# Kernel optimization log

Measured on AMD Instinct MI355X. Metric: run time of the kernel, lower is better.

Reference implementation:

```python
import jax, jax.numpy as jnp
import numpy as np

MAX_GRAD = 200.0
N_BLOCKS = 8

@jax.custom_jvp
def sqrt_bound(x):
    return jnp.sqrt(x)

@sqrt_bound.defjvp
def _sqrt_bound_jvp(primals, tangents):
    (x,), (xd,) = primals, tangents
    clipped = jnp.maximum(x, 1.0 / (4.0 * MAX_GRAD * MAX_GRAD))
    return jnp.sqrt(x), xd / (2.0 * jnp.sqrt(clipped))

def block_diag_linear(x, W, b):
    # x: [B,S,Din], W: [n_blocks, Din/n, Dout/n], b: [Dout]
    B, S, Din = x.shape
    n, blk_in, blk_out = W.shape
    xb = x.reshape(B, S, n, blk_in)
    y = jnp.einsum('bsnh,nhd->bsnd', xb, W).reshape(B, S, n * blk_out)
    return y + b

def _scan_combine(c1, c2):
    a1r, a1i, x1r, x1i = c1
    a2r, a2i, x2r, x2i = c2
    ar = a2r * a1r - a2i * a1i
    ai = a2r * a1i + a2i * a1r
    xr = a2r * x1r - a2i * x1i + x2r
    xi = a2r * x1i + a2i * x1r + x2i
    return (ar, ai, xr, xi)

def rglru_forward(x, a_real_param, a_imag_param, W_in, b_in, Wg_x, bg_x, Wg_a, bg_a, W_out, b_out):
    # x: [B, S, d_in]
    x_h = jnp.einsum('bsd,dh->bsh', x, W_in) + b_in          # [B,S,d_hidden]
    gate_x = jax.nn.sigmoid(block_diag_linear(x_h, Wg_x, bg_x))  # [B,S,Dh]
    gate_a = jax.nn.sigmoid(block_diag_linear(x_h, Wg_a, bg_a))  # [B,S,Dh]
    log_a = -8.0 * gate_a * jax.nn.softplus(a_real_param)        # Re(log a)
    log_a_imag = a_imag_param * gate_a                           # Im(log a)
    mag = jnp.exp(log_a)
    a_re = mag * jnp.cos(log_a_imag)
    a_im = mag * jnp.sin(log_a_imag)
    a_sq = jnp.exp(2.0 * log_a)                                  # |a|^2
    Dh = log_a.shape[-1]
    # merged_to_complex: first half -> real part, second half -> imag part
    xr = x_h[..., :Dh]
    xi = x_h[..., Dh:]
    xr = gate_x * xr
    xi = gate_x * xi
    norm = sqrt_bound(1.0 - a_sq)                                # input normalization
    xr = norm * xr
    xi = norm * xi
    # linear recurrence h_t = a_t * h_{t-1} + x_t  (h0 = 0), parallel scan over seq axis
    _, _, hr, hi = jax.lax.associative_scan(_scan_combine, (a_re, a_im, xr, xi), axis=1)
    h = jnp.concatenate([hr, hi], axis=-1)                       # complex_to_merged
    h_last = jnp.concatenate([hr[:, -1], hi[:, -1]], axis=-1)    # [B, d_hidden]
    y = jnp.einsum('bsh,hd->bsd', h, W_out) + b_out              # Dense(d_in)
    return y, h_last

def setup_inputs() -> dict:
    key = jax.random.key(0)
    ks = jax.random.split(key, 10)
    B, S, d_in, d_hidden = 4, 4096, 2048, 2048
    Dh = d_hidden // 2
    blk_in, blk_out = d_hidden // N_BLOCKS, Dh // N_BLOCKS
    r_min, r_max, max_imag, eps = 0.9, 0.999, 0.1, 1e-8
    u1 = jax.random.uniform(ks[0], (Dh,))
    a_real = 0.5 * jnp.log(u1 * (r_max**2 - r_min**2) + r_min**2 + eps)
    a_real_param = jnp.log(jnp.exp(-a_real) - 1.0)
    a_imag_param = jnp.pi * max_imag * jax.random.uniform(ks[1], (Dh,))
    x = jax.random.normal(ks[2], (B, S, d_in), dtype=jnp.float32)
    W_in = jax.random.normal(ks[3], (d_in, d_hidden)) / np.sqrt(d_in)
    Wg_x = jax.random.normal(ks[4], (N_BLOCKS, blk_in, blk_out)) / np.sqrt(blk_in)
    Wg_a = jax.random.normal(ks[5], (N_BLOCKS, blk_in, blk_out)) / np.sqrt(blk_in)
    W_out = jax.random.normal(ks[6], (d_hidden, d_in)) / np.sqrt(d_hidden)
    return {
        'x': x,
        'a_real_param': a_real_param.astype(jnp.float32),
        'a_imag_param': a_imag_param.astype(jnp.float32),
        'W_in': W_in.astype(jnp.float32), 'b_in': jnp.zeros((d_hidden,), jnp.float32),
        'Wg_x': Wg_x.astype(jnp.float32), 'bg_x': jnp.zeros((Dh,), jnp.float32),
        'Wg_a': Wg_a.astype(jnp.float32), 'bg_a': jnp.zeros((Dh,), jnp.float32),
        'W_out': W_out.astype(jnp.float32), 'b_out': jnp.zeros((d_in,), jnp.float32),
    }

def reference(x, a_real_param, a_imag_param, W_in, b_in, Wg_x, bg_x, Wg_a, bg_a, W_out, b_out):
    return rglru_forward(x, a_real_param, a_imag_param, W_in, b_in, Wg_x, bg_x, Wg_a, bg_a, W_out, b_out)
```

## Files before the change

kernel.cpp:

```cpp
#include <hip/hip_runtime.h>
#include <hip/hip_bf16.h>


typedef unsigned short u16;
typedef unsigned int u32;
typedef unsigned long long u64;
typedef __attribute__((ext_vector_type(8))) short short8;
typedef __attribute__((ext_vector_type(4))) float floatx4;

#define DEV __device__ __forceinline__

DEV float bf2f(u16 u) { union { u32 i; float f; } v; v.i = ((u32)u) << 16; return v.f; }
DEV u16 f2bf(float f) {
  union { float f; u32 i; } v; v.f = f;
  u32 r = v.i + 0x7fffu + ((v.i >> 16) & 1u);
  return (u16)(r >> 16);
}
DEV float sigmoidf_(float x) { return 1.f / (1.f + __expf(-x)); }

#if __has_builtin(__builtin_amdgcn_global_load_lds)
#define USE_ASYNC_LDS 1
#endif

DEV void cp16(const void* g, void* l) {
#if defined(USE_ASYNC_LDS) && defined(__HIP_DEVICE_COMPILE__)
  __builtin_amdgcn_global_load_lds((const __attribute__((address_space(1))) u32*)g,
                                   (__attribute__((address_space(3))) u32*)l, 16, 0, 0);
#else
  *(short8*)l = *(const short8*)g;
#endif
}
#define WAIT_VM() asm volatile("s_waitcnt vmcnt(0)" ::: "memory")
#define LGKM0()  do { asm volatile("s_waitcnt lgkmcnt(0)" ::: "memory"); __builtin_amdgcn_sched_barrier(0); } while (0)
#define BAR()    __builtin_amdgcn_s_barrier()
#define VMC4()   asm volatile("s_waitcnt vmcnt(4)" ::: "memory")
#define SETP(p)  __builtin_amdgcn_s_setprio(p)

__global__ __launch_bounds__(256) void convert_f32_bf16(
    const float* __restrict__ src, u16* __restrict__ dst, long n) {
  long i = ((long)blockIdx.x * 256 + threadIdx.x) * 8;
  if (i >= n) return;
  float4 a = *(const float4*)(src + i);
  float4 b = *(const float4*)(src + i + 4);
  union { u16 u[8]; short8 v; } o;
  o.u[0] = f2bf(a.x); o.u[1] = f2bf(a.y); o.u[2] = f2bf(a.z); o.u[3] = f2bf(a.w);
  o.u[4] = f2bf(b.x); o.u[5] = f2bf(b.y); o.u[6] = f2bf(b.z); o.u[7] = f2bf(b.w);
  *(short8*)(dst + i) = o.v;
}

__global__ __launch_bounds__(256) void transpose_f32_bf16(
    const float* __restrict__ src, u16* __restrict__ dst, int R, int C,
    long sBatch, long dBatch) {
  __shared__ u16 tile[32][33];
  const int n = blockIdx.z;
  src += (long)n * sBatch;
  dst += (long)n * dBatch;
  const int c0 = blockIdx.x * 32, r0 = blockIdx.y * 32;
  const int tx = threadIdx.x, ty = threadIdx.y;
#pragma unroll
  for (int i = 0; i < 32; i += 8)
    tile[ty + i][tx] = f2bf(src[(long)(r0 + ty + i) * C + c0 + tx]);
  __syncthreads();
#pragma unroll
  for (int i = 0; i < 32; i += 8) dst[(long)(c0 + ty + i) * R + r0 + tx] = tile[tx][ty + i];
}

#define MQK(MH, NH)                                                                  \
  {                                                                                  \
    _Pragma("unroll") for (int mi = 0; mi < 4; ++mi)                                 \
        _Pragma("unroll") for (int nj = 0; nj < 2; ++nj)                             \
      acc[(MH)*4 + mi][(NH)*2 + nj] = __builtin_amdgcn_mfma_f32_16x16x32_bf16(       \
          af[(MH)*4 + mi][0], bf[(NH)*2 + nj][0], acc[(MH)*4 + mi][(NH)*2 + nj],     \
          0, 0, 0);                                                                  \
    _Pragma("unroll") for (int mi = 0; mi < 4; ++mi)                                 \
        _Pragma("unroll") for (int nj = 0; nj < 2; ++nj)                             \
      acc[(MH)*4 + mi][(NH)*2 + nj] = __builtin_amdgcn_mfma_f32_16x16x32_bf16(       \
          af[(MH)*4 + mi][1], bf[(NH)*2 + nj][1], acc[(MH)*4 + mi][(NH)*2 + nj],     \
          0, 0, 0);                                                                  \
  }

#define RDA(m0_, BO)                                                                 \
  {                                                                                  \
    _Pragma("unroll") for (int mi = (m0_); mi < (m0_) + 4; ++mi) {                   \
      af[mi][0] = *(const short8*)((const char*)SM + ((aRd0 ^ (BO)) + mi * 2048));   \
      af[mi][1] = *(const short8*)((const char*)SM + ((aRd1 ^ (BO)) + mi * 2048));   \
    }                                                                                \
  }
#define RDB(n0_, BO)                                                                 \
  {                                                                                  \
    _Pragma("unroll") for (int nj = (n0_); nj < (n0_) + 2; ++nj) {                   \
      bf[nj][0] = *(const short8*)((const char*)SM + ((bRd0 ^ (BO)) + nj * 2048));   \
      bf[nj][1] = *(const short8*)((const char*)SM + ((bRd1 ^ (BO)) + nj * 2048));   \
    }                                                                                \
  }

template <typename OutT, int KK>
__global__ __launch_bounds__(512, 2) void gemm256_bt_bias(
    const u16* __restrict__ A, const u16* __restrict__ BT,
    const float* __restrict__ bias, OutT* __restrict__ C, int M, int N) {
  constexpr int NT = KK >> 6;
  __shared__ __align__(16) u16 SM[65536];
  const int mt = M >> 8;
  const int cpx = gridDim.x >> 3;
  const int bid = blockIdx.x;
  const int wg = (bid & 7) * cpx + (bid >> 3);
  const int bm = wg % mt, bn = wg / mt;
  const int m0 = bm << 8, n0 = bn << 8;
  const int tid = threadIdx.x;
  const int lane = tid & 63, wid = tid >> 6;
  const int wr = wid >> 2, wc = wid & 3;
  const int lq = lane >> 4, lm = lane & 15;
  const int sz = lm & 7;

  u32 goffA0, goffA1, goffB0, goffB1;
  u32 lofA0, lofA1, lofB0, lofB1;
  {
    const int rowl = tid >> 3, gch = (tid & 7) ^ (rowl & 7);
    goffA0 = (u32)(((size_t)(m0 + rowl) * KK + (gch << 3)) * 2);
    goffA1 = (u32)(((size_t)(m0 + 128 + rowl) * KK + (gch << 3)) * 2);
    goffB0 = (u32)(((size_t)(n0 + rowl) * KK + (gch << 3)) * 2);
    goffB1 = (u32)(((size_t)(n0 + 128 + rowl) * KK + (gch << 3)) * 2);
    const u32 sl = (u32)tid * 16;
    lofA0 = sl; lofA1 = sl + 16384; lofB0 = sl + 65536; lofB1 = sl + 81920;
  }
  const u32 aRd0 = (u32)((((wr << 7) + lm) << 7) + ((lq ^ sz) << 4));
  const u32 aRd1 = aRd0 ^ 64u;
  const u32 bRd0 = (u32)(65536 + (((wc << 6) + lm) << 7) + ((lq ^ sz) << 4));
  const u32 bRd1 = bRd0 ^ 64u;

  auto stage2 = [&](u32 go, const char* base, u32 lo, u32 bo) {
    cp16(base + go, (char*)SM + (lo ^ bo));
    cp16(base + go + 64 * KK * 2, (char*)SM + ((lo ^ bo) + 8192));
  };
#define SBA(t) ((const char*)A + ((size_t)(t) << 7))
#define SBB(t) ((const char*)BT + ((size_t)(t) << 7))

  floatx4 acc[8][4];
#pragma unroll
  for (int i = 0; i < 8; ++i)
#pragma unroll
    for (int j = 0; j < 4; ++j) { acc[i][j].x = 0.f; acc[i][j].y = 0.f; acc[i][j].z = 0.f; acc[i][j].w = 0.f; }
  short8 af[8][2], bf[4][2];

  stage2(goffA0, SBA(0), lofA0, 0);
  stage2(goffB0, SBB(0), lofB0, 0);
  stage2(goffA1, SBA(0), lofA1, 0);
  stage2(goffB1, SBB(0), lofB1, 0);
  stage2(goffA0, SBA(1), lofA0, 0x8000u);
  stage2(goffB0, SBB(1), lofB0, 0x8000u);
  stage2(goffA1, SBA(1), lofA1, 0x8000u);
  asm volatile("s_waitcnt vmcnt(6)" ::: "memory");
  BAR();
  RDA(0, 0u);
  RDB(0, 0u);

  for (int T = 0; T < NT - 2; ++T) {
    const u32 bo = (u32)((T & 1) << 15), bq = bo ^ 0x8000u;
    stage2(goffB1, SBB(T + 1), lofB1, bq);
    BAR(); LGKM0();
    RDB(2, bo);
    SETP(1); MQK(0, 0); SETP(0);
    BAR();
    stage2(goffA0, SBA(T + 2), lofA0, bo);
    BAR(); LGKM0();
    RDA(4, bo);
    SETP(1); MQK(0, 1); SETP(0);
    VMC4();
    BAR();
    stage2(goffB0, SBB(T + 2), lofB0, bo);
    BAR(); LGKM0();
    RDA(0, bq);
    SETP(1); MQK(1, 0); SETP(0);
    VMC4();
    BAR();
    stage2(goffA1, SBA(T + 2), lofA1, bo);
    BAR(); LGKM0();
    RDB(0, bq);
    SETP(1); MQK(1, 1); SETP(0);
    BAR();
  }
  {
    const int T = NT - 2;
    const u32 bo = (u32)((T & 1) << 15), bq = bo ^ 0x8000u;
    stage2(goffB1, SBB(T + 1), lofB1, bq);
    BAR(); LGKM0(); RDB(2, bo); SETP(1); MQK(0, 0); SETP(0); BAR();
    BAR(); LGKM0(); RDA(4, bo); SETP(1); MQK(0, 1); SETP(0); WAIT_VM(); BAR();
    BAR(); LGKM0(); RDA(0, bq); SETP(1); MQK(1, 0); SETP(0); BAR();
    BAR(); LGKM0(); RDB(0, bq); SETP(1); MQK(1, 1); SETP(0); BAR();
  }
  {
    const u32 bo = (u32)(((NT - 1) & 1) << 15);
    BAR(); LGKM0(); RDB(2, bo); SETP(1); MQK(0, 0); SETP(0); BAR();
    BAR(); LGKM0(); RDA(4, bo); SETP(1); MQK(0, 1); SETP(0); BAR();
    BAR(); LGKM0(); SETP(1); MQK(1, 0); SETP(0); BAR();
    BAR(); LGKM0(); SETP(1); MQK(1, 1); SETP(0); BAR();
  }
#undef SBA
#undef SBB

  float bv[4];
#pragma unroll
  for (int nj = 0; nj < 4; ++nj) bv[nj] = bias[n0 + (wc << 6) + nj * 16 + lm];
  float* Cs = (float*)SM;
#pragma unroll
  for (int s = 0; s < 4; ++s) {
    __syncthreads();
    if (wr == (s >> 1)) {
#pragma unroll
      for (int mi2 = 0; mi2 < 4; ++mi2) {
        const int mi = ((s & 1) << 2) + mi2;
#pragma unroll
        for (int nj = 0; nj < 4; ++nj)
#pragma unroll
          for (int rr = 0; rr < 4; ++rr)
            Cs[(mi2 * 16 + lq * 4 + rr) * 260 + (wc << 6) + nj * 16 + lm] =
                acc[mi][nj][rr] + bv[nj];
      }
    }
    __syncthreads();
#pragma unroll
    for (int w = 0; w < 8; ++w) {
      int fi = (w << 9) + tid;
      int rl = fi >> 6, cc = fi & 63;
      float4 v = *(const float4*)&Cs[rl * 260 + (cc << 2)];
      size_t grow = (size_t)(m0 + (s << 6) + rl) * N + n0 + (cc << 2);
      if constexpr (sizeof(OutT) == 2) {
        union { u16 u[4]; u64 q; } o;
        o.u[0] = f2bf(v.x); o.u[1] = f2bf(v.y); o.u[2] = f2bf(v.z); o.u[3] = f2bf(v.w);
        *(u64*)((u16*)C + grow) = o.q;
      } else {
        *(float4*)((float*)C + grow) = v;
      }
    }
  }
}

__global__ __launch_bounds__(256, 2) void gate_elem_kernel(
    const u16* __restrict__ xh, const u16* __restrict__ wgt,
    const float* __restrict__ bgx, const float* __restrict__ bga,
    const float* __restrict__ arp,
    float* __restrict__ ga_out, u16* __restrict__ xr_out, u16* __restrict__ xi_out) {
  __shared__ __align__(16) u16 As[128 * 64];
  __shared__ __align__(16) u16 Bs[256 * 64];

  const int m0 = blockIdx.x << 7;
  const int blk = blockIdx.y;
  const int tid = threadIdx.x;
  const int lane = tid & 63, wid = tid >> 6;
  const int wm = (wid & 1) << 6, wn = (wid >> 1) << 6;
  const int lq = lane >> 4, lm = lane & 15;

  floatx4 acc[4][8];
#pragma unroll
  for (int i = 0; i < 4; ++i)
#pragma unroll
    for (int j = 0; j < 8; ++j) { acc[i][j].x = 0.f; acc[i][j].y = 0.f; acc[i][j].z = 0.f; acc[i][j].w = 0.f; }

  const u16* Ag = xh + (size_t)m0 * 2048 + blk * 256;
  const u16* Bg = wgt + (size_t)blk * 65536;

  for (int kt = 0; kt < 256; kt += 64) {
#pragma unroll
    for (int j = 0; j < 4; ++j) {
      int slot = (j << 8) + tid;
      int row = slot >> 3, ch = slot & 7;
      int gch = ch ^ (row & 7);
      cp16(Ag + (size_t)row * 2048 + kt + (gch << 3), (char*)As + slot * 16);
    }
#pragma unroll
    for (int j = 0; j < 8; ++j) {
      int slot = (j << 8) + tid;
      int row = slot >> 3, ch = slot & 7;
      int gch = ch ^ (row & 7);
      cp16(Bg + (size_t)row * 256 + kt + (gch << 3), (char*)Bs + slot * 16);
    }
    WAIT_VM();
    __syncthreads();
#pragma unroll
    for (int kk = 0; kk < 64; kk += 32) {
      const int lc = (kk >> 3) + lq;
      short8 af[4], bfr[8];
#pragma unroll
      for (int mi = 0; mi < 4; ++mi) {
        int r = wm + mi * 16 + lm;
        af[mi] = *(const short8*)&As[r * 64 + ((lc ^ (r & 7)) << 3)];
      }
#pragma unroll
      for (int ni = 0; ni < 8; ++ni) {
        int r = (ni < 4) ? (wn + ni * 16 + lm) : (128 + wn + (ni - 4) * 16 + lm);
        bfr[ni] = *(const short8*)&Bs[r * 64 + ((lc ^ (r & 7)) << 3)];
      }
#pragma unroll
      for (int mi = 0; mi < 4; ++mi)
#pragma unroll
        for (int ni = 0; ni < 8; ++ni)
          acc[mi][ni] = __builtin_amdgcn_mfma_f32_16x16x32_bf16(af[mi], bfr[ni], acc[mi][ni], 0, 0, 0);
    }
    __syncthreads();
  }

#pragma unroll
  for (int ni = 0; ni < 4; ++ni) {
    const int c = (blk << 7) + wn + ni * 16 + lm;
    const float bxv = bgx[c], bav = bga[c];
    const float sp = log1pf(__expf(arp[c]));
#pragma unroll
    for (int mi = 0; mi < 4; ++mi) {
      const size_t rowg0 = (size_t)m0 + wm + mi * 16 + lq * 4;
#pragma unroll
      for (int r = 0; r < 4; ++r) {
        const size_t rowg = rowg0 + r;
        float gxv = sigmoidf_(acc[mi][ni][r] + bxv);
        float gav = sigmoidf_(acc[mi][ni + 4][r] + bav);
        float mag = __expf(-8.f * gav * sp);
        float norm = sqrtf(fmaxf(1.f - mag * mag, 0.f));
        float f = norm * gxv;
        ga_out[rowg * 1024 + c] = gav;
        xr_out[rowg * 1024 + c] = f2bf(f * bf2f(xh[rowg * 2048 + c]));
        xi_out[rowg * 1024 + c] = f2bf(f * bf2f(xh[rowg * 2048 + 1024 + c]));
      }
    }
  }
}

__global__ __launch_bounds__(256) void scan_pass1(
    const float* __restrict__ ga, const u16* __restrict__ xr, const u16* __restrict__ xi,
    const float* __restrict__ arp, const float* __restrict__ aip,
    float* __restrict__ Ar, float* __restrict__ Ai,
    float* __restrict__ Xr, float* __restrict__ Xi) {
  int tid = blockIdx.x * 256 + threadIdx.x;
  int c = tid & 1023;
  int chunk = (tid >> 10) & 63;
  int b = tid >> 16;
  float sp = log1pf(__expf(arp[c]));
  float aim = aip[c];
  size_t base = ((size_t)b * 4096 + chunk * 64) * 1024 + c;
  float Arr = 1.f, Aii = 0.f, Xrr = 0.f, Xii = 0.f;
#pragma unroll 4
  for (int i = 0; i < 64; ++i) {
    size_t idx = base + (size_t)i * 1024;
    float g = ga[idx];
    float mag = __expf(-8.f * g * sp);
    float s, co;
    __sincosf(aim * g, &s, &co);
    float ar = mag * co, ai = mag * s;
    float nxr = ar * Xrr - ai * Xii + bf2f(xr[idx]);
    float nxi = ar * Xii + ai * Xrr + bf2f(xi[idx]);
    Xrr = nxr; Xii = nxi;
    float nar = ar * Arr - ai * Aii;
    float nai = ar * Aii + ai * Arr;
    Arr = nar; Aii = nai;
  }
  Ar[tid] = Arr; Ai[tid] = Aii; Xr[tid] = Xrr; Xi[tid] = Xii;
}

__global__ __launch_bounds__(256) void scan_pass2(
    const float* __restrict__ Ar, const float* __restrict__ Ai,
    const float* __restrict__ Xr, const float* __restrict__ Xi,
    float* __restrict__ Hr, float* __restrict__ Hi) {
  int tid = blockIdx.x * 256 + threadIdx.x;
  int c = tid & 1023, b = tid >> 10;
  float hr = 0.f, hi = 0.f;
  for (int j = 0; j < 64; ++j) {
    int idx = (b << 16) + (j << 10) + c;
    Hr[idx] = hr; Hi[idx] = hi;
    float ar = Ar[idx], ai = Ai[idx];
    float nhr = ar * hr - ai * hi + Xr[idx];
    float nhi = ar * hi + ai * hr + Xi[idx];
    hr = nhr; hi = nhi;
  }
}

__global__ __launch_bounds__(256) void scan_pass3(
    const float* __restrict__ ga, const u16* __restrict__ xr, const u16* __restrict__ xi,
    const float* __restrict__ arp, const float* __restrict__ aip,
    const float* __restrict__ Hr, const float* __restrict__ Hi,
    u16* __restrict__ h_out, float* __restrict__ tail) {
  int tid = blockIdx.x * 256 + threadIdx.x;
  int c = tid & 1023;
  int chunk = (tid >> 10) & 63;
  int b = tid >> 16;
  float sp = log1pf(__expf(arp[c]));
  float aim = aip[c];
  size_t row0 = (size_t)b * 4096 + chunk * 64;
  size_t base = row0 * 1024 + c;
  float hr = Hr[tid], hi = Hi[tid];
#pragma unroll 4
  for (int i = 0; i < 64; ++i) {
    size_t idx = base + (size_t)i * 1024;
    float g = ga[idx];
    float mag = __expf(-8.f * g * sp);
    float s, co;
    __sincosf(aim * g, &s, &co);
    float ar = mag * co, ai = mag * s;
    float nhr = ar * hr - ai * hi + bf2f(xr[idx]);
    float nhi = ar * hi + ai * hr + bf2f(xi[idx]);
    hr = nhr; hi = nhi;
    size_t r = row0 + i;
    h_out[r * 2048 + c] = f2bf(hr);
    h_out[r * 2048 + 1024 + c] = f2bf(hi);
  }
  if (chunk == 63) {
    tail[(size_t)b * 2048 + c] = hr;
    tail[(size_t)b * 2048 + 1024 + c] = hi;
  }
}

static const size_t OFF_XH = 0;
static const size_t OFF_GA = 67108864;
static const size_t OFF_XR = 134217728;
static const size_t OFF_XI = 167772160;
static const size_t OFF_WIT = 201326592;
static const size_t OFF_WOT = 209715200;
static const size_t OFF_WGT = 218103808;
static const size_t OFF_AGR = 219152384;
static const size_t OFF_AGI = 220200960;
static const size_t OFF_AXR = 221249536;
static const size_t OFF_AXI = 222298112;
static const size_t OFF_HPR = 223346688;
static const size_t OFF_HPI = 224395264;

extern "C" void kernel_launch(void* const* d_in, const int* in_sizes, int n_in,
                              void* d_out, int out_size, void* d_ws, size_t ws_size,
                              hipStream_t stream) {
  const float* x    = (const float*)d_in[0];
  const float* arp  = (const float*)d_in[1];
  const float* aip  = (const float*)d_in[2];
  const float* W_in = (const float*)d_in[3];
  const float* b_in = (const float*)d_in[4];
  const float* Wg_x = (const float*)d_in[5];
  const float* bg_x = (const float*)d_in[6];
  const float* Wg_a = (const float*)d_in[7];
  const float* bg_a = (const float*)d_in[8];
  const float* W_out = (const float*)d_in[9];
  const float* b_out = (const float*)d_in[10];

  char* ws = (char*)d_ws;
  u16* XH = (u16*)(ws + OFF_XH);
  u16* XB = (u16*)(ws + OFF_GA);
  float* GA = (float*)(ws + OFF_GA);
  u16* XR = (u16*)(ws + OFF_XR);
  u16* XI = (u16*)(ws + OFF_XI);
  u16* WIT = (u16*)(ws + OFF_WIT);
  u16* WOT = (u16*)(ws + OFF_WOT);
  u16* WGT = (u16*)(ws + OFF_WGT);
  float* AGR = (float*)(ws + OFF_AGR);
  float* AGI = (float*)(ws + OFF_AGI);
  float* AXR = (float*)(ws + OFF_AXR);
  float* AXI = (float*)(ws + OFF_AXI);
  float* HPR = (float*)(ws + OFF_HPR);
  float* HPI = (float*)(ws + OFF_HPI);

  float* y_out = (float*)d_out;
  float* h_last = (float*)d_out + (size_t)16384 * 2048;

  convert_f32_bf16<<<16384, 256, 0, stream>>>(x, XB, (long)16384 * 2048);

  dim3 tb(32, 8);
  transpose_f32_bf16<<<dim3(64, 64, 1), tb, 0, stream>>>(W_in, WIT, 2048, 2048, 0, 0);
  transpose_f32_bf16<<<dim3(64, 64, 1), tb, 0, stream>>>(W_out, WOT, 2048, 2048, 0, 0);
  transpose_f32_bf16<<<dim3(4, 8, 8), tb, 0, stream>>>(Wg_x, WGT, 256, 128, 32768, 65536);
  transpose_f32_bf16<<<dim3(4, 8, 8), tb, 0, stream>>>(Wg_a, WGT + 32768, 256, 128, 32768, 65536);

  gemm256_bt_bias<u16, 2048><<<512, 512, 0, stream>>>(XB, WIT, b_in, XH, 16384, 2048);
  gate_elem_kernel<<<dim3(128, 8), 256, 0, stream>>>(XH, WGT, bg_x, bg_a, arp, GA, XR, XI);
  scan_pass1<<<1024, 256, 0, stream>>>(GA, XR, XI, arp, aip, AGR, AGI, AXR, AXI);
  scan_pass2<<<16, 256, 0, stream>>>(AGR, AGI, AXR, AXI, HPR, HPI);
  scan_pass3<<<1024, 256, 0, stream>>>(GA, XR, XI, arp, aip, HPR, HPI, XH , h_last);
  gemm256_bt_bias<float, 2048><<<512, 512, 0, stream>>>(XH, WOT, b_out, y_out, 16384, 2048);
}
```

Before: 706.9 us.

## Vectorize scan passes, stage gate epilogue through LDS, interleave MFMA scheduling

Several changes at once. The GEMM main loop gets sched_group_barrier hints that interleave MFMA and LDS-read instructions. The gate kernel epilogue now stages per-tile results through shared memory so global stores and the xh loads become row-contiguous float4/u64 accesses instead of scattered 2-byte and 4-byte ones. scan_pass1 and scan_pass3 each handle two channels per thread with wider loads and stores and launch half as many blocks. scan_pass2 is relaunched with 64-thread blocks so its work spreads over more CUs. Together these target memory-access inefficiency, at the cost of extra barriers in the epilogue and fewer threads in the scans.

```diff
diff --git a/kernel.cpp b/kernel.cpp
--- a/kernel.cpp
+++ b/kernel.cpp
@@ -35,6 +35,12 @@
 #define BAR()    __builtin_amdgcn_s_barrier()
 #define VMC4()   asm volatile("s_waitcnt vmcnt(4)" ::: "memory")
 #define SETP(p)  __builtin_amdgcn_s_setprio(p)
+#define SGB(m, n) __builtin_amdgcn_sched_group_barrier(m, n, 0)
+
+template <int R> DEV void sgbIL() {
+#pragma unroll
+  for (int i = 0; i < R; ++i) { SGB(0x100, 1); SGB(0x8, 16 / R); }
+}
 
 __global__ __launch_bounds__(256) void convert_f32_bf16(
     const float* __restrict__ src, u16* __restrict__ dst, long n) {
@@ -160,23 +166,27 @@
     BAR(); LGKM0();
     RDB(2, bo);
     SETP(1); MQK(0, 0); SETP(0);
+    sgbIL<4>();
     BAR();
     stage2(goffA0, SBA(T + 2), lofA0, bo);
     BAR(); LGKM0();
     RDA(4, bo);
     SETP(1); MQK(0, 1); SETP(0);
+    sgbIL<8>();
     VMC4();
     BAR();
     stage2(goffB0, SBB(T + 2), lofB0, bo);
     BAR(); LGKM0();
     RDA(0, bq);
     SETP(1); MQK(1, 0); SETP(0);
+    sgbIL<8>();
     VMC4();
     BAR();
     stage2(goffA1, SBA(T + 2), lofA1, bo);
     BAR(); LGKM0();
     RDB(0, bq);
     SETP(1); MQK(1, 1); SETP(0);
+    sgbIL<4>();
     BAR();
   }
   {
@@ -299,26 +309,52 @@
     __syncthreads();
   }
 
+  float* fs = (float*)As;
+  float* gas = (float*)Bs;
+  float bxv[4], bav[4], spv[4];
 #pragma unroll
   for (int ni = 0; ni < 4; ++ni) {
     const int c = (blk << 7) + wn + ni * 16 + lm;
-    const float bxv = bgx[c], bav = bga[c];
-    const float sp = log1pf(__expf(arp[c]));
-#pragma unroll
-    for (int mi = 0; mi < 4; ++mi) {
-      const size_t rowg0 = (size_t)m0 + wm + mi * 16 + lq * 4;
-#pragma unroll
-      for (int r = 0; r < 4; ++r) {
-        const size_t rowg = rowg0 + r;
-        float gxv = sigmoidf_(acc[mi][ni][r] + bxv);
-        float gav = sigmoidf_(acc[mi][ni + 4][r] + bav);
-        float mag = __expf(-8.f * gav * sp);
-        float norm = sqrtf(fmaxf(1.f - mag * mag, 0.f));
-        float f = norm * gxv;
-        ga_out[rowg * 1024 + c] = gav;
-        xr_out[rowg * 1024 + c] = f2bf(f * bf2f(xh[rowg * 2048 + c]));
-        xi_out[rowg * 1024 + c] = f2bf(f * bf2f(xh[rowg * 2048 + 1024 + c]));
-      }
+    bxv[ni] = bgx[c]; bav[ni] = bga[c];
+    spv[ni] = log1pf(__expf(arp[c]));
+  }
+  const int blkc = blk << 7;
+#pragma unroll
+  for (int s = 0; s < 8; ++s) {
+    __syncthreads();
+    if (wm == ((s >= 4) ? 64 : 0)) {
+      const int mi = s & 3;
+#pragma unroll
+      for (int ni = 0; ni < 4; ++ni)
+#pragma unroll
+        for (int r = 0; r < 4; ++r) {
+          float gxv = sigmoidf_(acc[mi][ni][r] + bxv[ni]);
+          float gav = sigmoidf_(acc[mi][ni + 4][r] + bav[ni]);
+          float mag = __expf(-8.f * gav * spv[ni]);
+          float norm = sqrtf(fmaxf(1.f - mag * mag, 0.f));
+          const int rw = lq * 4 + r, cw = wn + ni * 16 + lm;
+          fs[rw * 132 + cw] = norm * gxv;
+          gas[rw * 132 + cw] = gav;
+        }
+    }
+    __syncthreads();
+#pragma unroll
+    for (int w = 0; w < 2; ++w) {
+      const int q = (w << 8) + tid;
+      const int row = q >> 5, c4 = (q & 31) << 2;
+      const size_t rowg = (size_t)m0 + s * 16 + row;
+      const float4 fv = *(const float4*)&fs[row * 132 + c4];
+      const float4 gv = *(const float4*)&gas[row * 132 + c4];
+      *(float4*)&ga_out[rowg * 1024 + blkc + c4] = gv;
+      union { u16 u[4]; u64 q8; } xa, xb, oa, ob;
+      xa.q8 = *(const u64*)&xh[rowg * 2048 + blkc + c4];
+      xb.q8 = *(const u64*)&xh[rowg * 2048 + 1024 + blkc + c4];
+      oa.u[0] = f2bf(fv.x * bf2f(xa.u[0])); oa.u[1] = f2bf(fv.y * bf2f(xa.u[1]));
+      oa.u[2] = f2bf(fv.z * bf2f(xa.u[2])); oa.u[3] = f2bf(fv.w * bf2f(xa.u[3]));
+      ob.u[0] = f2bf(fv.x * bf2f(xb.u[0])); ob.u[1] = f2bf(fv.y * bf2f(xb.u[1]));
+      ob.u[2] = f2bf(fv.z * bf2f(xb.u[2])); ob.u[3] = f2bf(fv.w * bf2f(xb.u[3]));
+      *(u64*)&xr_out[rowg * 1024 + blkc + c4] = oa.q8;
+      *(u64*)&xi_out[rowg * 1024 + blkc + c4] = ob.q8;
     }
   }
 }
@@ -328,37 +364,50 @@
     const float* __restrict__ arp, const float* __restrict__ aip,
     float* __restrict__ Ar, float* __restrict__ Ai,
     float* __restrict__ Xr, float* __restrict__ Xi) {
-  int tid = blockIdx.x * 256 + threadIdx.x;
-  int c = tid & 1023;
-  int chunk = (tid >> 10) & 63;
-  int b = tid >> 16;
-  float sp = log1pf(__expf(arp[c]));
-  float aim = aip[c];
-  size_t base = ((size_t)b * 4096 + chunk * 64) * 1024 + c;
-  float Arr = 1.f, Aii = 0.f, Xrr = 0.f, Xii = 0.f;
+  int t = blockIdx.x * 256 + threadIdx.x;
+  int c2 = (t & 511) << 1;
+  int chunk = (t >> 9) & 63;
+  int b = t >> 15;
+  float2 sp, am;
+  sp.x = log1pf(__expf(arp[c2])); sp.y = log1pf(__expf(arp[c2 + 1]));
+  am.x = aip[c2]; am.y = aip[c2 + 1];
+  size_t base = ((size_t)b * 4096 + chunk * 64) * 1024 + c2;
+  float Ar0 = 1.f, Ai0 = 0.f, Xr0 = 0.f, Xi0 = 0.f;
+  float Ar1 = 1.f, Ai1 = 0.f, Xr1 = 0.f, Xi1 = 0.f;
 #pragma unroll 4
   for (int i = 0; i < 64; ++i) {
     size_t idx = base + (size_t)i * 1024;
-    float g = ga[idx];
-    float mag = __expf(-8.f * g * sp);
-    float s, co;
-    __sincosf(aim * g, &s, &co);
-    float ar = mag * co, ai = mag * s;
-    float nxr = ar * Xrr - ai * Xii + bf2f(xr[idx]);
-    float nxi = ar * Xii + ai * Xrr + bf2f(xi[idx]);
-    Xrr = nxr; Xii = nxi;
-    float nar = ar * Arr - ai * Aii;
-    float nai = ar * Aii + ai * Arr;
-    Arr = nar; Aii = nai;
-  }
-  Ar[tid] = Arr; Ai[tid] = Aii; Xr[tid] = Xrr; Xi[tid] = Xii;
+    float2 g = *(const float2*)&ga[idx];
+    union { u32 w; u16 u[2]; } vr, vi;
+    vr.w = *(const u32*)&xr[idx];
+    vi.w = *(const u32*)&xi[idx];
+    { float mag = __expf(-8.f * g.x * sp.x); float s, co; __sincosf(am.x * g.x, &s, &co);
+      float ar = mag * co, ai = mag * s;
+      float nxr = ar * Xr0 - ai * Xi0 + bf2f(vr.u[0]);
+      float nxi = ar * Xi0 + ai * Xr0 + bf2f(vi.u[0]);
+      Xr0 = nxr; Xi0 = nxi;
+      float nar = ar * Ar0 - ai * Ai0, nai = ar * Ai0 + ai * Ar0;
+      Ar0 = nar; Ai0 = nai; }
+    { float mag = __expf(-8.f * g.y * sp.y); float s, co; __sincosf(am.y * g.y, &s, &co);
+      float ar = mag * co, ai = mag * s;
+      float nxr = ar * Xr1 - ai * Xi1 + bf2f(vr.u[1]);
+      float nxi = ar * Xi1 + ai * Xr1 + bf2f(vi.u[1]);
+      Xr1 = nxr; Xi1 = nxi;
+      float nar = ar * Ar1 - ai * Ai1, nai = ar * Ai1 + ai * Ar1;
+      Ar1 = nar; Ai1 = nai; }
+  }
+  int o = ((b << 6) + chunk) << 10;
+  *(float2*)&Ar[o + c2] = make_float2(Ar0, Ar1);
+  *(float2*)&Ai[o + c2] = make_float2(Ai0, Ai1);
+  *(float2*)&Xr[o + c2] = make_float2(Xr0, Xr1);
+  *(float2*)&Xi[o + c2] = make_float2(Xi0, Xi1);
 }
 
 __global__ __launch_bounds__(256) void scan_pass2(
     const float* __restrict__ Ar, const float* __restrict__ Ai,
     const float* __restrict__ Xr, const float* __restrict__ Xi,
     float* __restrict__ Hr, float* __restrict__ Hi) {
-  int tid = blockIdx.x * 256 + threadIdx.x;
+  int tid = blockIdx.x * 64 + threadIdx.x;
   int c = tid & 1023, b = tid >> 10;
   float hr = 0.f, hi = 0.f;
   for (int j = 0; j < 64; ++j) {
@@ -376,33 +425,45 @@
     const float* __restrict__ arp, const float* __restrict__ aip,
     const float* __restrict__ Hr, const float* __restrict__ Hi,
     u16* __restrict__ h_out, float* __restrict__ tail) {
-  int tid = blockIdx.x * 256 + threadIdx.x;
-  int c = tid & 1023;
-  int chunk = (tid >> 10) & 63;
-  int b = tid >> 16;
-  float sp = log1pf(__expf(arp[c]));
-  float aim = aip[c];
+  int t = blockIdx.x * 256 + threadIdx.x;
+  int c2 = (t & 511) << 1;
+  int chunk = (t >> 9) & 63;
+  int b = t >> 15;
+  float2 sp, am;
+  sp.x = log1pf(__expf(arp[c2])); sp.y = log1pf(__expf(arp[c2 + 1]));
+  am.x = aip[c2]; am.y = aip[c2 + 1];
   size_t row0 = (size_t)b * 4096 + chunk * 64;
-  size_t base = row0 * 1024 + c;
-  float hr = Hr[tid], hi = Hi[tid];
+  size_t base = row0 * 1024 + c2;
+  int o = ((b << 6) + chunk) << 10;
+  float2 h0 = *(const float2*)&Hr[o + c2];
+  float2 h1 = *(const float2*)&Hi[o + c2];
+  float hr0 = h0.x, hr1 = h0.y, hi0 = h1.x, hi1 = h1.y;
 #pragma unroll 4
   for (int i = 0; i < 64; ++i) {
     size_t idx = base + (size_t)i * 1024;
-    float g = ga[idx];
-    float mag = __expf(-8.f * g * sp);
-    float s, co;
-    __sincosf(aim * g, &s, &co);
-    float ar = mag * co, ai = mag * s;
-    float nhr = ar * hr - ai * hi + bf2f(xr[idx]);
-    float nhi = ar * hi + ai * hr + bf2f(xi[idx]);
-    hr = nhr; hi = nhi;
+    float2 g = *(const float2*)&ga[idx];
+    union { u32 w; u16 u[2]; } vr, vi, w0, w1;
+    vr.w = *(const u32*)&xr[idx];
+    vi.w = *(const u32*)&xi[idx];
+    { float mag = __expf(-8.f * g.x * sp.x); float s, co; __sincosf(am.x * g.x, &s, &co);
+      float ar = mag * co, ai = mag * s;
+      float nhr = ar * hr0 - ai * hi0 + bf2f(vr.u[0]);
+      float nhi = ar * hi0 + ai * hr0 + bf2f(vi.u[0]);
+      hr0 = nhr; hi0 = nhi; }
+    { float mag = __expf(-8.f * g.y * sp.y); float s, co; __sincosf(am.y * g.y, &s, &co);
+      float ar = mag * co, ai = mag * s;
+      float nhr = ar * hr1 - ai * hi1 + bf2f(vr.u[1]);
+      float nhi = ar * hi1 + ai * hr1 + bf2f(vi.u[1]);
+      hr1 = nhr; hi1 = nhi; }
     size_t r = row0 + i;
-    h_out[r * 2048 + c] = f2bf(hr);
-    h_out[r * 2048 + 1024 + c] = f2bf(hi);
+    w0.u[0] = f2bf(hr0); w0.u[1] = f2bf(hr1);
+    w1.u[0] = f2bf(hi0); w1.u[1] = f2bf(hi1);
+    *(u32*)&h_out[r * 2048 + c2] = w0.w;
+    *(u32*)&h_out[r * 2048 + 1024 + c2] = w1.w;
   }
   if (chunk == 63) {
-    tail[(size_t)b * 2048 + c] = hr;
-    tail[(size_t)b * 2048 + 1024 + c] = hi;
+    *(float2*)&tail[(size_t)b * 2048 + c2] = make_float2(hr0, hr1);
+    *(float2*)&tail[(size_t)b * 2048 + 1024 + c2] = make_float2(hi0, hi1);
   }
 }
 
@@ -464,8 +525,8 @@
 
   gemm256_bt_bias<u16, 2048><<<512, 512, 0, stream>>>(XB, WIT, b_in, XH, 16384, 2048);
   gate_elem_kernel<<<dim3(128, 8), 256, 0, stream>>>(XH, WGT, bg_x, bg_a, arp, GA, XR, XI);
-  scan_pass1<<<1024, 256, 0, stream>>>(GA, XR, XI, arp, aip, AGR, AGI, AXR, AXI);
-  scan_pass2<<<16, 256, 0, stream>>>(AGR, AGI, AXR, AXI, HPR, HPI);
-  scan_pass3<<<1024, 256, 0, stream>>>(GA, XR, XI, arp, aip, HPR, HPI, XH , h_last);
+  scan_pass1<<<512, 256, 0, stream>>>(GA, XR, XI, arp, aip, AGR, AGI, AXR, AXI);
+  scan_pass2<<<64, 64, 0, stream>>>(AGR, AGI, AXR, AXI, HPR, HPI);
+  scan_pass3<<<512, 256, 0, stream>>>(GA, XR, XI, arp, aip, HPR, HPI, XH , h_last);
   gemm256_bt_bias<float, 2048><<<512, 512, 0, stream>>>(XH, WOT, b_out, y_out, 16384, 2048);
 }
```

New measurement: 670.4 us. 5.2% less time.
